# Optimization experiments

Measured on AMD Instinct MI355X. Metric: run time of the kernel, lower is better.

Reference implementation:

```python
import jax, jax.numpy as jnp
import numpy as np

BN_EPS = 1e-5


def _conv1x1(x, W, b):
    # x: (B, Cin, H, W), W: (Cout, Cin), b: (Cout,)
    return jnp.einsum('bchw,oc->bohw', x, W) + b[None, :, None, None]


def _bn(x, gamma, beta, mean, var):
    # inference-mode BatchNorm2d with running stats
    inv = gamma / jnp.sqrt(var + BN_EPS)
    return x * inv[None, :, None, None] + (beta - mean * inv)[None, :, None, None]


def setup_inputs() -> dict:
    key = jax.random.key(0)
    ks = jax.random.split(key, 8)
    B, N, C, H, W = 4, 3, 256, 48, 48
    Ck = C // 2  # key/query/value channels (scale=2)
    s = 0.02
    return {
        'x': jax.random.normal(ks[0], (B, N, C, H, W), jnp.float32),
        # f_key / f_query (shared): conv1x1 + BN
        'Wk': jax.random.normal(ks[1], (Ck, C), jnp.float32) * s,
        'bk': jnp.zeros((Ck,), jnp.float32),
        'gk': jnp.ones((Ck,), jnp.float32),
        'betak': jnp.zeros((Ck,), jnp.float32),
        'mk': jnp.zeros((Ck,), jnp.float32),
        'vk': jnp.ones((Ck,), jnp.float32),
        # f_value
        'Wv': jax.random.normal(ks[2], (Ck, C), jnp.float32) * s,
        'bv': jnp.zeros((Ck,), jnp.float32),
        # f_out
        'Wo': jax.random.normal(ks[3], (C, Ck), jnp.float32) * s,
        'bo': jnp.zeros((C,), jnp.float32),
        # fuse_layer: in = 2*C, out = C
        'Wf': jax.random.normal(ks[4], (C, 2 * C), jnp.float32) * s,
        'bf': jnp.zeros((C,), jnp.float32),
    }


def reference(x, Wk, bk, gk, betak, mk, vk, Wv, bv, Wo, bo, Wf, bf):
    B, N, C, H, W = x.shape  # N == 3
    HW = H * W
    Ck = Wk.shape[0]
    scale = Ck ** (-0.5)

    # Precompute shared key/query and value features for all 3 views
    xf = x.reshape(B * N, C, H, W)
    k_all = _bn(_conv1x1(xf, Wk, bk), gk, betak, mk, vk).reshape(B, N, Ck, HW)
    v_all = _conv1x1(xf, Wv, bv).reshape(B, N, Ck, HW)

    outs = []
    attn_maps = []
    for i in range(3):  # fixed small structural loop over views
        adj_ids = [j for j in range(3) if j != i]
        ref = x[:, i]                          # (B, C, H, W)
        q = k_all[:, i].transpose(0, 2, 1)     # (B, HW, Ck)  f_query == f_key
        matching = jnp.zeros_like(ref)
        for j in adj_ids:
            sim = jnp.einsum('bqc,bck->bqk', q, k_all[:, j]) * scale  # (B, HW, HW)
            attn = jax.nn.softmax(sim, axis=-1)
            ctx = jnp.einsum('bqk,bck->bcq', attn, v_all[:, j])       # (B, Ck, HW)
            ctx = ctx.reshape(B, Ck, H, W)
            matching = matching + _conv1x1(ctx, Wo, bo)
            if i == 0:
                attn_maps.append(attn)
        fuse = _conv1x1(jnp.concatenate([ref, matching], axis=1), Wf, bf)
        outs.append(ref + fuse)

    out = jnp.stack(outs, axis=1)                    # (B, 3, C, H, W)
    attention_maps = jnp.stack(attn_maps, axis=1)    # (B, 2, HW, HW)
    return out, attention_maps
```

## Files before the change

kernel.cpp:

```cpp
#include <hip/hip_runtime.h>

typedef short s8v __attribute__((ext_vector_type(8)));
typedef short s4v __attribute__((ext_vector_type(4)));
typedef float f4v __attribute__((ext_vector_type(4)));
typedef unsigned u32v2 __attribute__((ext_vector_type(2)));
typedef unsigned short u16;

#define MFMA(a,b,c) __builtin_amdgcn_mfma_f32_16x16x32_bf16(a,b,c,0,0,0)

__device__ __forceinline__ float bf2f(u16 x){
  unsigned u = ((unsigned)x) << 16;
  return __builtin_bit_cast(float, u);
}
__device__ __forceinline__ u16 f2bf(float f){
  unsigned u = __builtin_bit_cast(unsigned, f);
  u += 0x7FFFu + ((u >> 16) & 1u);
  return (u16)(u >> 16);
}

__device__ __forceinline__ void gload16(const void* g, void* l){
  __builtin_amdgcn_global_load_lds((const __attribute__((address_space(1))) unsigned*)g,
                                   (__attribute__((address_space(3))) unsigned*)l, 16, 0, 0);
}
__device__ __forceinline__ void nt_store4(float* p, f4v v){
  __builtin_nontemporal_store(v, (f4v*)p);
}

#define CC   256
#define CK   128
#define HW   2304
#define NF   12
#define C2E  0.1275174996992022f
#define OFF_KT   0u
#define OFF_V    7077888u
#define OFF_CTX  14155776u
#define OFF_RS   42467328u
#define OFF_PAR  42909696u
#define OFF_WK16 42911744u
#define OFF_WV16 42977280u
#define OFF_WF16 43042816u
#define OFF_WCMB 43304960u

__global__ void k0_params(const float* __restrict__ Wkf, const float* __restrict__ Wvf,
                          const float* __restrict__ bk, const float* __restrict__ gk,
                          const float* __restrict__ betak, const float* __restrict__ mk,
                          const float* __restrict__ vk, const float* __restrict__ Wo,
                          const float* __restrict__ Wf, const float* __restrict__ bo,
                          const float* __restrict__ bfv,
                          u16* __restrict__ Wk16, u16* __restrict__ Wv16, u16* __restrict__ Wf16,
                          float* kscale, float* kbias, float* btot, u16* Wcomb){
  int c = blockIdx.x;
  int o = threadIdx.x;
  int gid = c*256 + o;
  Wk16[gid] = f2bf(Wkf[gid]);
  Wv16[gid] = f2bf(Wvf[gid]);
  {
    f4v wf4 = *(const f4v*)(Wf + (size_t)gid*4);
    #pragma unroll
    for(int u=0;u<4;u++) Wf16[(size_t)gid*4+u] = f2bf(wf4[u]);
  }
  float acc = 0.f;
  for(int m=0;m<256;m++)
    acc += Wf[(size_t)o*512 + 256 + m] * Wo[(size_t)m*128 + c];
  Wcomb[(size_t)o*128 + c] = f2bf(acc);
  if (c == 0){
    float a2 = 0.f;
    for(int m=0;m<256;m++)
      a2 += Wf[(size_t)o*512 + 256 + m] * bo[m];
    btot[o] = bfv[o] + 2.0f*a2;
    if (o < 128){
      float inv = gk[o] * rsqrtf(vk[o] + 1e-5f);
      kscale[o] = inv;
      kbias[o]  = betak[o] + (bk[o] - mk[o])*inv;
    }
  }
}

__device__ __forceinline__ void stage_xt(const float* __restrict__ xf, int pb, int tid, char* xt){
  #pragma unroll
  for(int it=0; it<16; ++it){
    int idx = tid + 256*it;
    int c = idx>>4, slot = idx&15;
    f4v v = *(const f4v*)(xf + (size_t)c*HW + pb + slot*4);
    #pragma unroll
    for(int u=0;u<4;u++){
      int p = slot*4+u;
      *(u16*)(xt + p*512 + ((2*c) ^ ((p&7)<<4))) = f2bf(v[u]);
    }
  }
}
__device__ __forceinline__ s8v xt_frag(const char* xt, int r, int kt, int g){
  return *(const s8v*)(xt + r*512 + (((unsigned)(64*kt+16*g)) ^ ((unsigned)(r&7)<<4)));
}

__global__ __launch_bounds__(256) void k1_kv(const float* __restrict__ x, const u16* __restrict__ Wk,
                                             const u16* __restrict__ Wv, const float* __restrict__ bv,
                                             const float* __restrict__ kscale, const float* __restrict__ kbias,
                                             u16* __restrict__ kT, u16* __restrict__ vout){
  int f  = blockIdx.y;
  int pb = blockIdx.x*64;
  int tid = threadIdx.x;
  int w = tid>>6, l = tid&63, s = l&15, g = l>>4;
  __shared__ char xt[32768];
  stage_xt(x + (size_t)f*CC*HW, pb, tid, xt);
  __syncthreads();
  {
    s8v afr[8];
    #pragma unroll
    for(int kt=0;kt<8;kt++) afr[kt] = xt_frag(xt, 16*w+s, kt, g);
    f4v acc[8] = {};
    #pragma unroll
    for(int kt=0;kt<8;kt++){
      #pragma unroll
      for(int nt=0;nt<8;nt++){
        s8v b = *(const s8v*)(Wk + (size_t)(16*nt+s)*CC + 32*kt + 8*g);
        acc[nt] = MFMA(afr[kt], b, acc[nt]);
      }
    }
    u16* kout = kT + (size_t)f*HW*CK;
    int q0 = pb + 16*w;
    #pragma unroll
    for(int nt=0;nt<8;nt++){
      int o = 16*nt + s;
      float sc = kscale[o], bi = kbias[o];
      #pragma unroll
      for(int r=0;r<4;r++){
        int q = q0 + 4*g + r;
        kout[(size_t)q*CK + o] = f2bf(acc[nt][r]*sc + bi);
      }
    }
  }
  {
    s8v afr[2][8];
    #pragma unroll
    for(int mt=0;mt<2;mt++)
      #pragma unroll
      for(int kt=0;kt<8;kt++)
        afr[mt][kt] = *(const s8v*)(Wv + (size_t)(32*w+16*mt+s)*CC + 32*kt + 8*g);
    f4v acc[2][4] = {};
    #pragma unroll
    for(int kt=0;kt<8;kt++){
      #pragma unroll
      for(int nt=0;nt<4;nt++){
        s8v b = xt_frag(xt, 16*nt+s, kt, g);
        #pragma unroll
        for(int mt=0;mt<2;mt++)
          acc[mt][nt] = MFMA(afr[mt][kt], b, acc[mt][nt]);
      }
    }
    u16* vf = vout + (size_t)f*CK*HW;
    #pragma unroll
    for(int mt=0;mt<2;mt++){
      #pragma unroll
      for(int r=0;r<4;r++){
        int o = 32*w + 16*mt + 4*g + r;
        float bvo = bv[o];
        #pragma unroll
        for(int nt=0;nt<4;nt++)
          vf[(size_t)o*HW + pb + 16*nt + s] = f2bf(acc[mt][nt][r] + bvo);
      }
    }
  }
}

__global__ __launch_bounds__(256, 2) void k2_attn(const u16* __restrict__ kT, const u16* __restrict__ v,
                                                  u16* __restrict__ ctxS, float* __restrict__ rs){
  int qb  = blockIdx.x;
  int yy  = blockIdx.y;
  int bij = yy>>1, half = yy&1;
  int b = bij/6, r6_ = bij - 6*b, i = r6_>>1, jj = r6_&1;
  int adj0 = (i==0) ? 1 : 0;
  int adj1 = (i==2) ? 1 : 2;
  int j = jj ? adj1 : adj0;
  int tid = threadIdx.x;
  int w = tid>>6, l = tid&63, s = l&15, g = l>>4;
  int q0 = qb*128 + w*32;

  __shared__ char L[81920];
  char* plw = L + 65536 + w*4096;

  const u16* kTi = kT + (size_t)(b*3+i)*HW*CK;
  const u16* kTj = kT + (size_t)(b*3+j)*HW*CK;
  const u16* vj  = v  + (size_t)(b*3+j)*CK*HW;

  s8v qfr[2][4];
  #pragma unroll
  for(int qf=0;qf<2;qf++)
    #pragma unroll
    for(int kt=0;kt<4;kt++)
      qfr[qf][kt] = *(const s8v*)(kTi + (size_t)(q0+16*qf+s)*CK + 32*kt + 8*g);

  f4v ctx[8][2] = {};
  float psum[2] = {0.f, 0.f};

  auto STAGE = [&](int p0, int buf){
    const char* kbase = (const char*)kTj + (size_t)p0*256;
    const char* vbase = (const char*)vj  + (size_t)p0*2;
    char* lK = L + buf*16384 + w*1024;
    char* lV = L + 32768 + buf*16384 + w*1024;
    #pragma unroll
    for(int it=0; it<4; ++it){
      unsigned Lo = (unsigned)tid*16u + (unsigned)it*4096u;
      unsigned Gs = Lo ^ (((Lo>>8)&7u)<<4);
      gload16(kbase + Gs, lK + it*4096);
      unsigned row = Lo>>7;
      unsigned col = (Lo & 127u) ^ ((row&7u)<<4);
      gload16(vbase + (size_t)row*(HW*2) + col, lV + it*4096);
    }
  };

  int pbase = half*18;
  STAGE(pbase*64, 0);
  __syncthreads();
  int cur = 0;

  for(int pt=0; pt<18; ++pt){
    int p0 = (pbase + pt)*64;
    if (pt < 17) STAGE(p0+64, cur^1);
    const char* lK = L + cur*16384;
    const char* lV = L + 32768 + cur*16384;

    f4v sa[2][4] = {};
    #pragma unroll
    for(int kt=0;kt<4;kt++){
      #pragma unroll
      for(int nt=0;nt<4;nt++){
        unsigned row = (unsigned)(16*nt + s);
        unsigned cb  = ((unsigned)(64*kt + 16*g)) ^ ((row&7u)<<4);
        s8v kfr = *(const s8v*)(lK + row*256 + cb);
        #pragma unroll
        for(int qf=0;qf<2;qf++) sa[qf][nt] = MFMA(kfr, qfr[qf][kt], sa[qf][nt]);
      }
    }
    #pragma unroll
    for(int qf=0;qf<2;qf++){
      #pragma unroll
      for(int nt=0;nt<4;nt++){
        float e0 = exp2f(sa[qf][nt][0]*C2E);
        float e1 = exp2f(sa[qf][nt][1]*C2E);
        float e2 = exp2f(sa[qf][nt][2]*C2E);
        float e3 = exp2f(sa[qf][nt][3]*C2E);
        psum[qf] += (e0+e1)+(e2+e3);
        u32v2 pk;
        pk[0] = (unsigned)f2bf(e0) | ((unsigned)f2bf(e1)<<16);
        pk[1] = (unsigned)f2bf(e2) | ((unsigned)f2bf(e3)<<16);
        unsigned off = ((unsigned)(32*nt + 8*g)) ^ ((unsigned)(s&7)<<4);
        *(u32v2*)(plw + (unsigned)qf*2048u + (unsigned)s*128u + off) = pk;
      }
    }
    s8v pf[2][2];
    #pragma unroll
    for(int qf=0;qf<2;qf++)
      #pragma unroll
      for(int kt=0;kt<2;kt++)
        pf[qf][kt] = *(const s8v*)(plw + (unsigned)qf*2048u + (unsigned)s*128u +
                                   (((unsigned)(64*kt + 16*g)) ^ ((unsigned)(s&7)<<4)));
    #pragma unroll
    for(int kt=0;kt<2;kt++){
      #pragma unroll
      for(int ct=0;ct<8;ct++){
        unsigned row = (unsigned)(16*ct + s);
        unsigned cb  = ((unsigned)(64*kt + 16*g)) ^ ((row&7u)<<4);
        s8v vfr = *(const s8v*)(lV + row*128 + cb);
        #pragma unroll
        for(int qf=0;qf<2;qf++) ctx[ct][qf] = MFMA(vfr, pf[qf][kt], ctx[ct][qf]);
      }
    }
    __syncthreads();
    cur ^= 1;
  }

  #pragma unroll
  for(int qf=0;qf<2;qf++){
    float xsum = psum[qf];
    xsum += __shfl_xor(xsum, 16);
    xsum += __shfl_xor(xsum, 32);
    if (l < 16)
      rs[(size_t)yy*HW + q0 + 16*qf + s] = xsum;
  }
  u16* cS = ctxS + (size_t)yy*HW*CK;
  #pragma unroll
  for(int qf=0;qf<2;qf++){
    #pragma unroll
    for(int ct=0;ct<8;ct++){
      s4v pk;
      #pragma unroll
      for(int r=0;r<4;r++) pk[r] = (short)f2bf(ctx[ct][qf][r]);
      *(s4v*)(cS + (size_t)(q0+16*qf+s)*CK + 16*ct + 4*g) = pk;
    }
  }
}

__global__ __launch_bounds__(256) void k2c_attnmap(const u16* __restrict__ kT,
                                                   const float* __restrict__ rs,
                                                   float* __restrict__ attn_out){
  int qb = blockIdx.x;
  int y  = blockIdx.y;
  int plane = y>>1, ph = y&1;
  int b = plane>>1, jj = plane&1, j = jj + 1;
  int tid = threadIdx.x;
  int w = tid>>6, l = tid&63, s = l&15, g = l>>4;
  int q0 = qb*64 + w*16;

  __shared__ char  ldsK[16384];
  __shared__ float ptile[4][16][68];
  __shared__ float inv16[4][16];

  const u16* kTi = kT + (size_t)(b*3)*HW*CK;
  const u16* kTj = kT + (size_t)(b*3+j)*HW*CK;

  s8v qf[4];
  #pragma unroll
  for(int kt=0;kt<4;kt++) qf[kt] = *(const s8v*)(kTi + (size_t)(q0+s)*CK + 32*kt + 8*g);

  {
    f4v ra = *(const f4v*)(rs + (size_t)(12*b+2*jj  )*HW + q0 + 4*g);
    f4v rb = *(const f4v*)(rs + (size_t)(12*b+2*jj+1)*HW + q0 + 4*g);
    if (s == 0){
      #pragma unroll
      for(int r=0;r<4;r++) inv16[w][4*g+r] = 1.0f / (ra[r] + rb[r]);
    }
  }
  __syncthreads();

  float* ao = attn_out + (size_t)plane*HW*HW;

  for(int pt=ph*18; pt<ph*18+18; ++pt){
    int p0 = pt*64;
    {
      const char* kbase = (const char*)kTj + (size_t)p0*256;
      char* lK = (char*)ldsK + w*1024;
      #pragma unroll
      for(int it=0; it<4; ++it){
        unsigned Lo = (unsigned)tid*16u + (unsigned)it*4096u;
        unsigned Gs = Lo ^ (((Lo>>8)&7u)<<4);
        gload16(kbase + Gs, lK + it*4096);
      }
    }
    __syncthreads();

    f4v sa[4] = {};
    #pragma unroll
    for(int kt=0;kt<4;kt++){
      #pragma unroll
      for(int nt=0;nt<4;nt++){
        unsigned row = (unsigned)(16*nt + s);
        unsigned cb  = ((unsigned)(64*kt + 16*g)) ^ ((row&7u)<<4);
        s8v bfr = *(const s8v*)((const char*)ldsK + row*256 + cb);
        sa[nt] = MFMA(qf[kt], bfr, sa[nt]);
      }
    }
    #pragma unroll
    for(int r=0;r<4;r++){
      #pragma unroll
      for(int nt=0;nt<4;nt++)
        ptile[w][4*g+r][16*nt+s] = exp2f(sa[nt][r]*C2E);
    }
    #pragma unroll
    for(int pass=0; pass<4; ++pass){
      int row = 4*pass + g;
      float inv = inv16[w][row];
      f4v val = *(const f4v*)&ptile[w][row][4*s];
      #pragma unroll
      for(int u=0;u<4;u++) val[u] *= inv;
      nt_store4(ao + (size_t)(q0+row)*HW + p0 + 4*s, val);
    }
    __syncthreads();
  }
}

__global__ __launch_bounds__(256) void k3_out(const float* __restrict__ x,
                                              const u16* __restrict__ Wf, const u16* __restrict__ Wcomb,
                                              const float* __restrict__ btot, const u16* __restrict__ ctxS,
                                              const float* __restrict__ rs,
                                              float* __restrict__ out){
  int f = blockIdx.y, pb = blockIdx.x*64;
  int tid = threadIdx.x;
  int w = tid>>6, l = tid&63, s = l&15, g = l>>4;
  __shared__ char xt[32768];
  const float* xf = x + (size_t)f*CC*HW;
  stage_xt(xf, pb, tid, xt);
  __syncthreads();
  f4v acc[4][4] = {};
  #pragma unroll
  for(int kt=0;kt<8;kt++){
    s8v bfr[4];
    #pragma unroll
    for(int nt=0;nt<4;nt++) bfr[nt] = xt_frag(xt, 16*nt+s, kt, g);
    #pragma unroll
    for(int mt=0;mt<4;mt++){
      s8v a = *(const s8v*)(Wf + (size_t)(64*w+16*mt+s)*512 + 32*kt + 8*g);
      #pragma unroll
      for(int nt=0;nt<4;nt++) acc[mt][nt] = MFMA(a, bfr[nt], acc[mt][nt]);
    }
  }
  #pragma unroll
  for(int jj=0;jj<2;jj++){
    const u16* cA = ctxS + (size_t)(4*f+2*jj  )*HW*CK;
    const u16* cB = ctxS + (size_t)(4*f+2*jj+1)*HW*CK;
    f4v acc2[4][4] = {};
    #pragma unroll
    for(int kt=0;kt<4;kt++){
      s8v b0[4], b1[4];
      #pragma unroll
      for(int nt=0;nt<4;nt++){
        b0[nt] = *(const s8v*)(cA + (size_t)(pb+16*nt+s)*CK + 32*kt + 8*g);
        b1[nt] = *(const s8v*)(cB + (size_t)(pb+16*nt+s)*CK + 32*kt + 8*g);
      }
      #pragma unroll
      for(int mt=0;mt<4;mt++){
        s8v a = *(const s8v*)(Wcomb + (size_t)(64*w+16*mt+s)*CK + 32*kt + 8*g);
        #pragma unroll
        for(int nt=0;nt<4;nt++){
          acc2[mt][nt] = MFMA(a, b0[nt], acc2[mt][nt]);
          acc2[mt][nt] = MFMA(a, b1[nt], acc2[mt][nt]);
        }
      }
    }
    const float* rA = rs + (size_t)(4*f+2*jj  )*HW;
    const float* rB = rs + (size_t)(4*f+2*jj+1)*HW;
    float invq[4];
    #pragma unroll
    for(int nt=0;nt<4;nt++){
      int q = pb + 16*nt + s;
      invq[nt] = 1.0f / (rA[q] + rB[q]);
    }
    #pragma unroll
    for(int mt=0;mt<4;mt++)
      #pragma unroll
      for(int nt=0;nt<4;nt++)
        #pragma unroll
        for(int r=0;r<4;r++) acc[mt][nt][r] += acc2[mt][nt][r]*invq[nt];
  }
  float* of = out + (size_t)f*CC*HW;
  #pragma unroll
  for(int mt=0;mt<4;mt++){
    #pragma unroll
    for(int r=0;r<4;r++){
      int o = 64*w + 16*mt + 4*g + r;
      float bb = btot[o];
      #pragma unroll
      for(int nt=0;nt<4;nt++){
        int p = pb + 16*nt + s;
        of[(size_t)o*HW + p] = acc[mt][nt][r] + bb + xf[(size_t)o*HW + p];
      }
    }
  }
}

extern "C" void kernel_launch(void* const* d_in, const int* in_sizes, int n_in,
                              void* d_out, int out_size, void* d_ws, size_t ws_size,
                              hipStream_t stream) {
  const float* x     = (const float*)d_in[0];
  const float* Wk    = (const float*)d_in[1];
  const float* bk    = (const float*)d_in[2];
  const float* gk    = (const float*)d_in[3];
  const float* betak = (const float*)d_in[4];
  const float* mk    = (const float*)d_in[5];
  const float* vk    = (const float*)d_in[6];
  const float* Wv    = (const float*)d_in[7];
  const float* bv    = (const float*)d_in[8];
  const float* Wo    = (const float*)d_in[9];
  const float* bo    = (const float*)d_in[10];
  const float* Wf    = (const float*)d_in[11];
  const float* bf    = (const float*)d_in[12];
  float* out = (float*)d_out;

  char* ws = (char*)d_ws;
  u16*   kT     = (u16*)(ws + OFF_KT);
  u16*   vv     = (u16*)(ws + OFF_V);
  u16*   ctxS   = (u16*)(ws + OFF_CTX);
  float* rs     = (float*)(ws + OFF_RS);
  float* kscale = (float*)(ws + OFF_PAR);
  float* kbias  = kscale + 128;
  float* btot   = kbias + 128;
  u16*   Wk16   = (u16*)(ws + OFF_WK16);
  u16*   Wv16   = (u16*)(ws + OFF_WV16);
  u16*   Wf16   = (u16*)(ws + OFF_WF16);
  u16*   Wcomb  = (u16*)(ws + OFF_WCMB);

  float* attn = out + (size_t)NF*CC*HW;

  k0_params<<<dim3(128), dim3(256), 0, stream>>>(Wk, Wv, bk, gk, betak, mk, vk, Wo, Wf, bo, bf,
                                                 Wk16, Wv16, Wf16, kscale, kbias, btot, Wcomb);
  k1_kv<<<dim3(36,12), dim3(256), 0, stream>>>(x, Wk16, Wv16, bv, kscale, kbias, kT, vv);
  k2_attn<<<dim3(18,48), dim3(256), 0, stream>>>(kT, vv, ctxS, rs);
  k2c_attnmap<<<dim3(36,16), dim3(256), 0, stream>>>(kT, rs, attn);
  k3_out<<<dim3(36,12), dim3(256), 0, stream>>>(x, Wf16, Wcomb, btot, ctxS, rs, out);
}
```

Baseline: 234.0 us.

## Merge attention-map and output kernels into one launch; use packed bf16 convert

```diff
diff --git a/kernel.cpp b/kernel.cpp
--- a/kernel.cpp
+++ b/kernel.cpp
@@ -16,6 +16,11 @@
   unsigned u = __builtin_bit_cast(unsigned, f);
   u += 0x7FFFu + ((u >> 16) & 1u);
   return (u16)(u >> 16);
+}
+__device__ __forceinline__ unsigned cvtpk(float lo, float hi){
+  unsigned r;
+  asm("v_cvt_pk_bf16_f32 %0, %1, %2" : "=v"(r) : "v"(lo), "v"(hi));
+  return r;
 }
 
 __device__ __forceinline__ void gload16(const void* g, void* l){
@@ -242,8 +247,8 @@
         float e3 = exp2f(sa[qf][nt][3]*C2E);
         psum[qf] += (e0+e1)+(e2+e3);
         u32v2 pk;
-        pk[0] = (unsigned)f2bf(e0) | ((unsigned)f2bf(e1)<<16);
-        pk[1] = (unsigned)f2bf(e2) | ((unsigned)f2bf(e3)<<16);
+        pk[0] = cvtpk(e0, e1);
+        pk[1] = cvtpk(e2, e3);
         unsigned off = ((unsigned)(32*nt + 8*g)) ^ ((unsigned)(s&7)<<4);
         *(u32v2*)(plw + (unsigned)qf*2048u + (unsigned)s*128u + off) = pk;
       }
@@ -283,167 +288,166 @@
   for(int qf=0;qf<2;qf++){
     #pragma unroll
     for(int ct=0;ct<8;ct++){
-      s4v pk;
-      #pragma unroll
-      for(int r=0;r<4;r++) pk[r] = (short)f2bf(ctx[ct][qf][r]);
-      *(s4v*)(cS + (size_t)(q0+16*qf+s)*CK + 16*ct + 4*g) = pk;
-    }
-  }
-}
-
-__global__ __launch_bounds__(256) void k2c_attnmap(const u16* __restrict__ kT,
-                                                   const float* __restrict__ rs,
-                                                   float* __restrict__ attn_out){
-  int qb = blockIdx.x;
-  int y  = blockIdx.y;
-  int plane = y>>1, ph = y&1;
-  int b = plane>>1, jj = plane&1, j = jj + 1;
+      u32v2 pk;
+      pk[0] = cvtpk(ctx[ct][qf][0], ctx[ct][qf][1]);
+      pk[1] = cvtpk(ctx[ct][qf][2], ctx[ct][qf][3]);
+      *(u32v2*)(cS + (size_t)(q0+16*qf+s)*CK + 16*ct + 4*g) = pk;
+    }
+  }
+}
+
+__global__ __launch_bounds__(256) void k23_fused(const float* __restrict__ x,
+                                                 const u16* __restrict__ Wf, const u16* __restrict__ Wcomb,
+                                                 const float* __restrict__ btot, const u16* __restrict__ ctxS,
+                                                 const float* __restrict__ rs, const u16* __restrict__ kT,
+                                                 float* __restrict__ out, float* __restrict__ attn_out){
+  __shared__ __align__(16) char Lsh[34048];
   int tid = threadIdx.x;
   int w = tid>>6, l = tid&63, s = l&15, g = l>>4;
-  int q0 = qb*64 + w*16;
-
-  __shared__ char  ldsK[16384];
-  __shared__ float ptile[4][16][68];
-  __shared__ float inv16[4][16];
-
-  const u16* kTi = kT + (size_t)(b*3)*HW*CK;
-  const u16* kTj = kT + (size_t)(b*3+j)*HW*CK;
-
-  s8v qf[4];
-  #pragma unroll
-  for(int kt=0;kt<4;kt++) qf[kt] = *(const s8v*)(kTi + (size_t)(q0+s)*CK + 32*kt + 8*g);
-
-  {
-    f4v ra = *(const f4v*)(rs + (size_t)(12*b+2*jj  )*HW + q0 + 4*g);
-    f4v rb = *(const f4v*)(rs + (size_t)(12*b+2*jj+1)*HW + q0 + 4*g);
-    if (s == 0){
-      #pragma unroll
-      for(int r=0;r<4;r++) inv16[w][4*g+r] = 1.0f / (ra[r] + rb[r]);
-    }
-  }
-  __syncthreads();
-
-  float* ao = attn_out + (size_t)plane*HW*HW;
-
-  for(int pt=ph*18; pt<ph*18+18; ++pt){
-    int p0 = pt*64;
+  int role = blockIdx.y;
+
+  if (role < 12){
+    int f = role, pb = blockIdx.x*64;
+    char* xt = Lsh;
+    const float* xf = x + (size_t)f*CC*HW;
+    stage_xt(xf, pb, tid, xt);
+    __syncthreads();
+    f4v acc[4][4] = {};
+    #pragma unroll
+    for(int kt=0;kt<8;kt++){
+      s8v bfr[4];
+      #pragma unroll
+      for(int nt=0;nt<4;nt++) bfr[nt] = xt_frag(xt, 16*nt+s, kt, g);
+      #pragma unroll
+      for(int mt=0;mt<4;mt++){
+        s8v a = *(const s8v*)(Wf + (size_t)(64*w+16*mt+s)*512 + 32*kt + 8*g);
+        #pragma unroll
+        for(int nt=0;nt<4;nt++) acc[mt][nt] = MFMA(a, bfr[nt], acc[mt][nt]);
+      }
+    }
+    #pragma unroll
+    for(int jj=0;jj<2;jj++){
+      const u16* cA = ctxS + (size_t)(4*f+2*jj  )*HW*CK;
+      const u16* cB = ctxS + (size_t)(4*f+2*jj+1)*HW*CK;
+      f4v acc2[4][4] = {};
+      #pragma unroll
+      for(int kt=0;kt<4;kt++){
+        s8v b0[4], b1[4];
+        #pragma unroll
+        for(int nt=0;nt<4;nt++){
+          b0[nt] = *(const s8v*)(cA + (size_t)(pb+16*nt+s)*CK + 32*kt + 8*g);
+          b1[nt] = *(const s8v*)(cB + (size_t)(pb+16*nt+s)*CK + 32*kt + 8*g);
+        }
+        #pragma unroll
+        for(int mt=0;mt<4;mt++){
+          s8v a = *(const s8v*)(Wcomb + (size_t)(64*w+16*mt+s)*CK + 32*kt + 8*g);
+          #pragma unroll
+          for(int nt=0;nt<4;nt++){
+            acc2[mt][nt] = MFMA(a, b0[nt], acc2[mt][nt]);
+            acc2[mt][nt] = MFMA(a, b1[nt], acc2[mt][nt]);
+          }
+        }
+      }
+      const float* rA = rs + (size_t)(4*f+2*jj  )*HW;
+      const float* rB = rs + (size_t)(4*f+2*jj+1)*HW;
+      float invq[4];
+      #pragma unroll
+      for(int nt=0;nt<4;nt++){
+        int q = pb + 16*nt + s;
+        invq[nt] = 1.0f / (rA[q] + rB[q]);
+      }
+      #pragma unroll
+      for(int mt=0;mt<4;mt++)
+        #pragma unroll
+        for(int nt=0;nt<4;nt++)
+          #pragma unroll
+          for(int r=0;r<4;r++) acc[mt][nt][r] += acc2[mt][nt][r]*invq[nt];
+    }
+    float* of = out + (size_t)f*CC*HW;
+    #pragma unroll
+    for(int mt=0;mt<4;mt++){
+      #pragma unroll
+      for(int r=0;r<4;r++){
+        int o = 64*w + 16*mt + 4*g + r;
+        float bb = btot[o];
+        #pragma unroll
+        for(int nt=0;nt<4;nt++){
+          int p = pb + 16*nt + s;
+          of[(size_t)o*HW + p] = acc[mt][nt][r] + bb + xf[(size_t)o*HW + p];
+        }
+      }
+    }
+  } else {
+    int idx = role - 12;
+    int qb = blockIdx.x;
+    int plane = idx>>1, ph = idx&1;
+    int b = plane>>1, jj = plane&1, j = jj + 1;
+    int q0 = qb*64 + w*16;
+
+    char*  ldsK  = Lsh;
+    float* ptile = (float*)(Lsh + 16384);
+    float* inv16 = (float*)(Lsh + 16384 + 17408);
+
+    const u16* kTi = kT + (size_t)(b*3)*HW*CK;
+    const u16* kTj = kT + (size_t)(b*3+j)*HW*CK;
+
+    s8v qf[4];
+    #pragma unroll
+    for(int kt=0;kt<4;kt++) qf[kt] = *(const s8v*)(kTi + (size_t)(q0+s)*CK + 32*kt + 8*g);
+
     {
-      const char* kbase = (const char*)kTj + (size_t)p0*256;
-      char* lK = (char*)ldsK + w*1024;
-      #pragma unroll
-      for(int it=0; it<4; ++it){
-        unsigned Lo = (unsigned)tid*16u + (unsigned)it*4096u;
-        unsigned Gs = Lo ^ (((Lo>>8)&7u)<<4);
-        gload16(kbase + Gs, lK + it*4096);
+      f4v ra = *(const f4v*)(rs + (size_t)(12*b+2*jj  )*HW + q0 + 4*g);
+      f4v rb = *(const f4v*)(rs + (size_t)(12*b+2*jj+1)*HW + q0 + 4*g);
+      if (s == 0){
+        #pragma unroll
+        for(int r=0;r<4;r++) inv16[w*16 + 4*g+r] = 1.0f / (ra[r] + rb[r]);
       }
     }
     __syncthreads();
 
-    f4v sa[4] = {};
-    #pragma unroll
-    for(int kt=0;kt<4;kt++){
-      #pragma unroll
-      for(int nt=0;nt<4;nt++){
-        unsigned row = (unsigned)(16*nt + s);
-        unsigned cb  = ((unsigned)(64*kt + 16*g)) ^ ((row&7u)<<4);
-        s8v bfr = *(const s8v*)((const char*)ldsK + row*256 + cb);
-        sa[nt] = MFMA(qf[kt], bfr, sa[nt]);
-      }
-    }
-    #pragma unroll
-    for(int r=0;r<4;r++){
-      #pragma unroll
-      for(int nt=0;nt<4;nt++)
-        ptile[w][4*g+r][16*nt+s] = exp2f(sa[nt][r]*C2E);
-    }
-    #pragma unroll
-    for(int pass=0; pass<4; ++pass){
-      int row = 4*pass + g;
-      float inv = inv16[w][row];
-      f4v val = *(const f4v*)&ptile[w][row][4*s];
-      #pragma unroll
-      for(int u=0;u<4;u++) val[u] *= inv;
-      nt_store4(ao + (size_t)(q0+row)*HW + p0 + 4*s, val);
-    }
-    __syncthreads();
-  }
-}
-
-__global__ __launch_bounds__(256) void k3_out(const float* __restrict__ x,
-                                              const u16* __restrict__ Wf, const u16* __restrict__ Wcomb,
-                                              const float* __restrict__ btot, const u16* __restrict__ ctxS,
-                                              const float* __restrict__ rs,
-                                              float* __restrict__ out){
-  int f = blockIdx.y, pb = blockIdx.x*64;
-  int tid = threadIdx.x;
-  int w = tid>>6, l = tid&63, s = l&15, g = l>>4;
-  __shared__ char xt[32768];
-  const float* xf = x + (size_t)f*CC*HW;
-  stage_xt(xf, pb, tid, xt);
-  __syncthreads();
-  f4v acc[4][4] = {};
-  #pragma unroll
-  for(int kt=0;kt<8;kt++){
-    s8v bfr[4];
-    #pragma unroll
-    for(int nt=0;nt<4;nt++) bfr[nt] = xt_frag(xt, 16*nt+s, kt, g);
-    #pragma unroll
-    for(int mt=0;mt<4;mt++){
-      s8v a = *(const s8v*)(Wf + (size_t)(64*w+16*mt+s)*512 + 32*kt + 8*g);
-      #pragma unroll
-      for(int nt=0;nt<4;nt++) acc[mt][nt] = MFMA(a, bfr[nt], acc[mt][nt]);
-    }
-  }
-  #pragma unroll
-  for(int jj=0;jj<2;jj++){
-    const u16* cA = ctxS + (size_t)(4*f+2*jj  )*HW*CK;
-    const u16* cB = ctxS + (size_t)(4*f+2*jj+1)*HW*CK;
-    f4v acc2[4][4] = {};
-    #pragma unroll
-    for(int kt=0;kt<4;kt++){
-      s8v b0[4], b1[4];
-      #pragma unroll
-      for(int nt=0;nt<4;nt++){
-        b0[nt] = *(const s8v*)(cA + (size_t)(pb+16*nt+s)*CK + 32*kt + 8*g);
-        b1[nt] = *(const s8v*)(cB + (size_t)(pb+16*nt+s)*CK + 32*kt + 8*g);
-      }
-      #pragma unroll
-      for(int mt=0;mt<4;mt++){
-        s8v a = *(const s8v*)(Wcomb + (size_t)(64*w+16*mt+s)*CK + 32*kt + 8*g);
+    float* ao = attn_out + (size_t)plane*HW*HW;
+
+    for(int pt=ph*18; pt<ph*18+18; ++pt){
+      int p0 = pt*64;
+      {
+        const char* kbase = (const char*)kTj + (size_t)p0*256;
+        char* lK = ldsK + w*1024;
+        #pragma unroll
+        for(int it=0; it<4; ++it){
+          unsigned Lo = (unsigned)tid*16u + (unsigned)it*4096u;
+          unsigned Gs = Lo ^ (((Lo>>8)&7u)<<4);
+          gload16(kbase + Gs, lK + it*4096);
+        }
+      }
+      __syncthreads();
+
+      f4v sa[4] = {};
+      #pragma unroll
+      for(int kt=0;kt<4;kt++){
         #pragma unroll
         for(int nt=0;nt<4;nt++){
-          acc2[mt][nt] = MFMA(a, b0[nt], acc2[mt][nt]);
-          acc2[mt][nt] = MFMA(a, b1[nt], acc2[mt][nt]);
+          unsigned row = (unsigned)(16*nt + s);
+          unsigned cb  = ((unsigned)(64*kt + 16*g)) ^ ((row&7u)<<4);
+          s8v bfr = *(const s8v*)((const char*)ldsK + row*256 + cb);
+          sa[nt] = MFMA(qf[kt], bfr, sa[nt]);
         }
       }
-    }
-    const float* rA = rs + (size_t)(4*f+2*jj  )*HW;
-    const float* rB = rs + (size_t)(4*f+2*jj+1)*HW;
-    float invq[4];
-    #pragma unroll
-    for(int nt=0;nt<4;nt++){
-      int q = pb + 16*nt + s;
-      invq[nt] = 1.0f / (rA[q] + rB[q]);
-    }
-    #pragma unroll
-    for(int mt=0;mt<4;mt++)
-      #pragma unroll
-      for(int nt=0;nt<4;nt++)
-        #pragma unroll
-        for(int r=0;r<4;r++) acc[mt][nt][r] += acc2[mt][nt][r]*invq[nt];
-  }
-  float* of = out + (size_t)f*CC*HW;
-  #pragma unroll
-  for(int mt=0;mt<4;mt++){
-    #pragma unroll
-    for(int r=0;r<4;r++){
-      int o = 64*w + 16*mt + 4*g + r;
-      float bb = btot[o];
-      #pragma unroll
-      for(int nt=0;nt<4;nt++){
-        int p = pb + 16*nt + s;
-        of[(size_t)o*HW + p] = acc[mt][nt][r] + bb + xf[(size_t)o*HW + p];
-      }
+      #pragma unroll
+      for(int r=0;r<4;r++){
+        #pragma unroll
+        for(int nt=0;nt<4;nt++)
+          ptile[(w*16 + 4*g+r)*68 + 16*nt+s] = exp2f(sa[nt][r]*C2E);
+      }
+      #pragma unroll
+      for(int pass=0; pass<4; ++pass){
+        int row = 4*pass + g;
+        float inv = inv16[w*16 + row];
+        f4v val = *(const f4v*)&ptile[(w*16 + row)*68 + 4*s];
+        #pragma unroll
+        for(int u=0;u<4;u++) val[u] *= inv;
+        nt_store4(ao + (size_t)(q0+row)*HW + p0 + 4*s, val);
+      }
+      __syncthreads();
     }
   }
 }
@@ -485,6 +489,5 @@
                                                  Wk16, Wv16, Wf16, kscale, kbias, btot, Wcomb);
   k1_kv<<<dim3(36,12), dim3(256), 0, stream>>>(x, Wk16, Wv16, bv, kscale, kbias, kT, vv);
   k2_attn<<<dim3(18,48), dim3(256), 0, stream>>>(kT, vv, ctxS, rs);
-  k2c_attnmap<<<dim3(36,16), dim3(256), 0, stream>>>(kT, rs, attn);
-  k3_out<<<dim3(36,12), dim3(256), 0, stream>>>(x, Wf16, Wcomb, btot, ctxS, rs, out);
-}
+  k23_fused<<<dim3(36,28), dim3(256), 0, stream>>>(x, Wf16, Wcomb, btot, ctxS, rs, kT, out, attn);
+}
```

After: 244.9 us. 4.7% more time.
